# Optimization experiments

Hardware: AMD Instinct MI355X
Metric: run time of the kernel (lower is better)

## Reference

```python
import jax, jax.numpy as jnp
import numpy as np

B, N, M, D = 64, 16384, 64, 512
EPS = 1e-16


def setup_inputs() -> dict:
    key = jax.random.key(0)
    k1, k2, k3, k4 = jax.random.split(key, 4)
    controller_output = jax.random.normal(k1, (B, D), dtype=jnp.float32)
    w_prev = jax.random.uniform(k2, (B, N), dtype=jnp.float32)
    memory = jax.random.normal(k3, (B, N, M), dtype=jnp.float32)
    W = jax.random.normal(k4, (M + 6, D), dtype=jnp.float32) * (1.0 / np.sqrt(D))
    b = jnp.zeros((M + 6,), dtype=jnp.float32)
    return {"controller_output": controller_output, "w_prev": w_prev,
            "memory": memory, "W": W, "b": b}


def reference(controller_output, w_prev, memory, W, b):
    # fc_read projection -> [B, M+6], split into k, beta, g, s, gamma
    o = controller_output @ W.T + b
    k = o[:, :M]                      # [B, M] content key
    beta = jax.nn.softplus(o[:, M:M + 1])        # [B, 1] key strength
    g = jax.nn.sigmoid(o[:, M + 1:M + 2])        # [B, 1] interpolation gate
    s = jax.nn.softmax(o[:, M + 2:M + 5], axis=1)  # [B, 3] shift weights
    gamma = 1.0 + jax.nn.softplus(o[:, M + 5:M + 6])  # [B, 1] sharpening

    # content addressing: cosine similarity between k and each memory row
    num = jnp.einsum('bm,bnm->bn', k, memory)                      # [B, N]
    denom = (jnp.linalg.norm(k, axis=1, keepdims=True)
             * jnp.linalg.norm(memory, axis=2) + EPS)              # [B, N]
    w_c = jax.nn.softmax(beta * (num / denom), axis=1)             # [B, N]

    # interpolation with previous weighting
    w_g = g * w_c + (1.0 - g) * w_prev                              # [B, N]

    # circular convolution shift over {-1, 0, +1}
    w_t = (s[:, 0:1] * jnp.roll(w_g, 1, axis=1)
           + s[:, 1:2] * w_g
           + s[:, 2:3] * jnp.roll(w_g, -1, axis=1))                 # [B, N]

    # sharpening
    w_pow = w_t ** gamma
    w = w_pow / (jnp.sum(w_pow, axis=1, keepdims=True) + EPS)       # [B, N]

    # read: weighted sum of memory rows
    r = jnp.einsum('bn,bnm->bm', w, memory)                         # [B, M]
    return (r, w)
```

## Files before the change

### kernel.cpp

```cpp
#include <hip/hip_runtime.h>
#include <math.h>

#define B 64
#define N 16384
#define MDIM 64
#define DDIM 512
#define EPSF 1e-16f

#define K_OFF      0
#define SCAL_OFF   (B*64)
#define SCORE_OFF  (SCAL_OFF + B*8)
#define PART_OFF   (SCORE_OFF + B*N)

__device__ __forceinline__ float rowsum16(float x) {
    float t;
    t = __int_as_float(__builtin_amdgcn_update_dpp(0, __float_as_int(x), 0x128, 0xF, 0xF, true)); x += t;
    t = __int_as_float(__builtin_amdgcn_update_dpp(0, __float_as_int(x), 0x124, 0xF, 0xF, true)); x += t;
    t = __int_as_float(__builtin_amdgcn_update_dpp(0, __float_as_int(x), 0x122, 0xF, 0xF, true)); x += t;
    t = __int_as_float(__builtin_amdgcn_update_dpp(0, __float_as_int(x), 0x121, 0xF, 0xF, true)); x += t;
    return x;
}

__global__ __launch_bounds__(256) void k1(const float* __restrict__ c,
                                          const float* __restrict__ W,
                                          const float* __restrict__ bias,
                                          float* __restrict__ ws) {
    int b = blockIdx.x;
    __shared__ float cs[DDIM];
    __shared__ float osh[72];
    int tid = threadIdx.x;
    for (int i = tid; i < DDIM; i += 256) cs[i] = c[b * DDIM + i];
    __syncthreads();
    int wave = tid >> 6, lane = tid & 63;
    for (int j = wave; j < MDIM + 6; j += 4) {
        const float* wr = W + (size_t)j * DDIM;
        float sum = 0.f;
        for (int d = lane; d < DDIM; d += 64) sum += cs[d] * wr[d];
        for (int off = 32; off > 0; off >>= 1) sum += __shfl_xor(sum, off);
        if (lane == 0) osh[j] = sum + bias[j];
    }
    __syncthreads();
    if (tid < 64) ws[K_OFF + b * 64 + tid] = osh[tid];
    if (wave == 0) {
        float v = osh[lane];
        float sq = v * v;
        for (int off = 32; off > 0; off >>= 1) sq += __shfl_xor(sq, off);
        if (lane == 0) {
            float kn = sqrtf(sq);
            float ob = osh[64], og = osh[65], os0 = osh[66], os1 = osh[67],
                  os2 = osh[68], ogm = osh[69];
            float beta  = fmaxf(ob, 0.f) + log1pf(expf(-fabsf(ob)));
            float g     = 1.f / (1.f + expf(-og));
            float mx    = fmaxf(os0, fmaxf(os1, os2));
            float e0 = expf(os0 - mx), e1 = expf(os1 - mx), e2 = expf(os2 - mx);
            float es = e0 + e1 + e2;
            float gamma = 1.f + fmaxf(ogm, 0.f) + log1pf(expf(-fabsf(ogm)));
            float* sc = ws + SCAL_OFF + b * 8;
            sc[0] = kn; sc[1] = beta; sc[2] = g;
            sc[3] = e0 / es; sc[4] = e1 / es; sc[5] = e2 / es;
            sc[6] = gamma;
        }
    }
}

__global__ __launch_bounds__(256) void k2(const float* __restrict__ mem,
                                          float* __restrict__ ws) {
    int b = blockIdx.x >> 5, chunk = blockIdx.x & 31;
    __shared__ float ks[64];
    __shared__ float kb[2];
    int tid = threadIdx.x;
    if (tid < 64) ks[tid] = ws[K_OFF + b * 64 + tid];
    if (tid == 64) kb[0] = ws[SCAL_OFF + b * 8 + 0];
    if (tid == 65) kb[1] = ws[SCAL_OFF + b * 8 + 1];
    __syncthreads();
    float kn = kb[0], beta = kb[1];
    int grp = tid >> 4, ll = tid & 15;
    float k0 = ks[ll * 4], k1v = ks[ll * 4 + 1], k2v = ks[ll * 4 + 2], k3v = ks[ll * 4 + 3];
    int row0 = chunk * 512;
    #pragma unroll 4
    for (int it = 0; it < 32; ++it) {
        int row = row0 + it * 16 + grp;
        float4 v = *reinterpret_cast<const float4*>(
            mem + ((size_t)b * N + row) * MDIM + ll * 4);
        float dot = v.x * k0 + v.y * k1v + v.z * k2v + v.w * k3v;
        float sq  = v.x * v.x + v.y * v.y + v.z * v.z + v.w * v.w;
        dot = rowsum16(dot);
        sq  = rowsum16(sq);
        if (ll == 0) {
            float denom = kn * sqrtf(sq) + EPSF;
            ws[SCORE_OFF + (size_t)b * N + row] = beta * (dot / denom);
        }
    }
}

__global__ __launch_bounds__(1024) void kw(const float* __restrict__ w_prev,
                                           const float* __restrict__ ws,
                                           float* __restrict__ w_out) {
    int b = blockIdx.x;
    __shared__ float wg[N];
    __shared__ float red[16];
    int tid = threadIdx.x, wave = tid >> 6, lane = tid & 63;
    const float* sc = ws + SCORE_OFF + (size_t)b * N;
    const float* sl = ws + SCAL_OFF + b * 8;
    float g = sl[2], s0 = sl[3], s1 = sl[4], s2 = sl[5], gamma = sl[6];
    const float* wp = w_prev + (size_t)b * N;

    float scv[16];
    float mx = -INFINITY;
    #pragma unroll
    for (int j = 0; j < 16; ++j) {
        scv[j] = sc[tid + 1024 * j];
        mx = fmaxf(mx, scv[j]);
    }
    #pragma unroll
    for (int off = 32; off > 0; off >>= 1) mx = fmaxf(mx, __shfl_xor(mx, off));
    if (lane == 0) red[wave] = mx;
    __syncthreads();
    mx = red[0];
    #pragma unroll
    for (int w2 = 1; w2 < 16; ++w2) mx = fmaxf(mx, red[w2]);
    __syncthreads();

    float s = 0.f;
    #pragma unroll
    for (int j = 0; j < 16; ++j) {
        scv[j] = __expf(scv[j] - mx);
        s += scv[j];
    }
    #pragma unroll
    for (int off = 32; off > 0; off >>= 1) s += __shfl_xor(s, off);
    if (lane == 0) red[wave] = s;
    __syncthreads();
    s = red[0];
    #pragma unroll
    for (int w2 = 1; w2 < 16; ++w2) s += red[w2];
    float inv = 1.f / s;
    __syncthreads();

    #pragma unroll
    for (int j = 0; j < 16; ++j) {
        int i = tid + 1024 * j;
        wg[i] = g * (scv[j] * inv) + (1.f - g) * wp[i];
    }
    __syncthreads();

    float pv[16];
    float sp = 0.f;
    #pragma unroll
    for (int j = 0; j < 16; ++j) {
        int i = tid + 1024 * j;
        float wt = s0 * wg[(i - 1) & (N - 1)] + s1 * wg[i] + s2 * wg[(i + 1) & (N - 1)];
        float p = __expf(gamma * __logf(wt));
        pv[j] = p;
        sp += p;
    }
    #pragma unroll
    for (int off = 32; off > 0; off >>= 1) sp += __shfl_xor(sp, off);
    if (lane == 0) red[wave] = sp;
    __syncthreads();
    float spTot = red[0];
    #pragma unroll
    for (int w2 = 1; w2 < 16; ++w2) spTot += red[w2];
    float invp = 1.f / (spTot + EPSF);

    #pragma unroll
    for (int j = 0; j < 16; ++j) {
        int i = tid + 1024 * j;
        w_out[(size_t)b * N + i] = pv[j] * invp;
    }
}

__global__ __launch_bounds__(256) void kr(const float* __restrict__ mem,
                                          const float* __restrict__ w,
                                          float* __restrict__ part) {
    int b = blockIdx.x >> 5, chunk = blockIdx.x & 31;
    int tid = threadIdx.x, grp = tid >> 4, ll = tid & 15;
    float4 acc = make_float4(0.f, 0.f, 0.f, 0.f);
    int row0 = chunk * 512;
    #pragma unroll 4
    for (int it = 0; it < 32; ++it) {
        int row = row0 + it * 16 + grp;
        float wv = w[(size_t)b * N + row];
        float4 v = *reinterpret_cast<const float4*>(
            mem + ((size_t)b * N + row) * MDIM + ll * 4);
        acc.x += wv * v.x; acc.y += wv * v.y; acc.z += wv * v.z; acc.w += wv * v.w;
    }
    __shared__ float lds[16][64];
    lds[grp][ll * 4 + 0] = acc.x;
    lds[grp][ll * 4 + 1] = acc.y;
    lds[grp][ll * 4 + 2] = acc.z;
    lds[grp][ll * 4 + 3] = acc.w;
    __syncthreads();
    if (tid < 64) {
        float sacc = 0.f;
        #pragma unroll
        for (int gi = 0; gi < 16; ++gi) sacc += lds[gi][tid];
        part[(size_t)blockIdx.x * 64 + tid] = sacc;
    }
}

__global__ __launch_bounds__(64) void krr(const float* __restrict__ part,
                                          float* __restrict__ r) {
    int b = blockIdx.x, m = threadIdx.x;
    float s = 0.f;
    #pragma unroll
    for (int c = 0; c < 32; ++c) s += part[((size_t)b * 32 + c) * 64 + m];
    r[b * 64 + m] = s;
}

extern "C" void kernel_launch(void* const* d_in, const int* in_sizes, int n_in,
                              void* d_out, int out_size, void* d_ws, size_t ws_size,
                              hipStream_t stream) {
    const float* c      = (const float*)d_in[0];
    const float* w_prev = (const float*)d_in[1];
    const float* mem    = (const float*)d_in[2];
    const float* W      = (const float*)d_in[3];
    const float* bias   = (const float*)d_in[4];
    float* out = (float*)d_out;
    float* r_out = out;
    float* w_out = out + B * MDIM;
    float* ws = (float*)d_ws;

    k1<<<B, 256, 0, stream>>>(c, W, bias, ws);
    k2<<<B * 32, 256, 0, stream>>>(mem, ws);
    kw<<<B, 1024, 0, stream>>>(w_prev, ws, w_out);
    kr<<<B * 32, 256, 0, stream>>>(mem, w_out, ws + PART_OFF);
    krr<<<B, 64, 0, stream>>>(ws + PART_OFF, r_out);
}
```

Baseline: 113.7 us.

## Split per-batch softmax/sharpen kernel into chunked multi-block passes with tiny reduction kernels

Replaces the single 64-block kw kernel (one 1024-thread block per batch with 64KB LDS) with a chunked scheme. k2 now emits per-chunk max/sum-exp partials, and kc merges them with an online-softmax combine. kwb computes the interpolation, shift and power over 2048 blocks using a haloed LDS tile, kpp reduces the power sums, and kr folds the final normalization into the read pass and rescales w in place. This spreads the serial per-batch work across many CUs, at the cost of two extra launches and an extra read-modify-write of w. It also raises the k2 and kr unroll factor to 8.

```diff
diff --git a/kernel.cpp b/kernel.cpp
--- a/kernel.cpp
+++ b/kernel.cpp
@@ -10,7 +10,11 @@
 #define K_OFF      0
 #define SCAL_OFF   (B*64)
 #define SCORE_OFF  (SCAL_OFF + B*8)
-#define PART_OFF   (SCORE_OFF + B*N)
+#define MS_OFF     (SCORE_OFF + B*N)
+#define MXI_OFF    (MS_OFF + B*64)
+#define PSUM_OFF   (MXI_OFF + B*2)
+#define INVP_OFF   (PSUM_OFF + B*32)
+#define PART_OFF   (INVP_OFF + B)
 
 __device__ __forceinline__ float rowsum16(float x) {
     float t;
@@ -67,19 +71,21 @@
                                           float* __restrict__ ws) {
     int b = blockIdx.x >> 5, chunk = blockIdx.x & 31;
     __shared__ float ks[64];
-    __shared__ float kb[2];
+    __shared__ float kb2[2];
+    __shared__ float scbuf[512];
     int tid = threadIdx.x;
     if (tid < 64) ks[tid] = ws[K_OFF + b * 64 + tid];
-    if (tid == 64) kb[0] = ws[SCAL_OFF + b * 8 + 0];
-    if (tid == 65) kb[1] = ws[SCAL_OFF + b * 8 + 1];
-    __syncthreads();
-    float kn = kb[0], beta = kb[1];
+    if (tid == 64) kb2[0] = ws[SCAL_OFF + b * 8 + 0];
+    if (tid == 65) kb2[1] = ws[SCAL_OFF + b * 8 + 1];
+    __syncthreads();
+    float kn = kb2[0], beta = kb2[1];
     int grp = tid >> 4, ll = tid & 15;
     float k0 = ks[ll * 4], k1v = ks[ll * 4 + 1], k2v = ks[ll * 4 + 2], k3v = ks[ll * 4 + 3];
     int row0 = chunk * 512;
-    #pragma unroll 4
+    #pragma unroll 8
     for (int it = 0; it < 32; ++it) {
-        int row = row0 + it * 16 + grp;
+        int lrow = it * 16 + grp;
+        int row = row0 + lrow;
         float4 v = *reinterpret_cast<const float4*>(
             mem + ((size_t)b * N + row) * MDIM + ll * 4);
         float dot = v.x * k0 + v.y * k1v + v.z * k2v + v.w * k3v;
@@ -87,110 +93,140 @@
         dot = rowsum16(dot);
         sq  = rowsum16(sq);
         if (ll == 0) {
-            float denom = kn * sqrtf(sq) + EPSF;
-            ws[SCORE_OFF + (size_t)b * N + row] = beta * (dot / denom);
-        }
-    }
-}
-
-__global__ __launch_bounds__(1024) void kw(const float* __restrict__ w_prev,
-                                           const float* __restrict__ ws,
+            float score = beta * (dot / (kn * sqrtf(sq) + EPSF));
+            ws[SCORE_OFF + (size_t)b * N + row] = score;
+            scbuf[lrow] = score;
+        }
+    }
+    __syncthreads();
+    if (tid < 64) {
+        float vr[8];
+        float m = -1e30f;
+        #pragma unroll
+        for (int j = 0; j < 8; ++j) {
+            vr[j] = scbuf[tid + 64 * j];
+            m = fmaxf(m, vr[j]);
+        }
+        #pragma unroll
+        for (int off = 32; off > 0; off >>= 1) m = fmaxf(m, __shfl_xor(m, off));
+        float s = 0.f;
+        #pragma unroll
+        for (int j = 0; j < 8; ++j) s += __expf(vr[j] - m);
+        #pragma unroll
+        for (int off = 32; off > 0; off >>= 1) s += __shfl_xor(s, off);
+        if (tid == 0) {
+            ws[MS_OFF + ((size_t)b * 32 + chunk) * 2]     = m;
+            ws[MS_OFF + ((size_t)b * 32 + chunk) * 2 + 1] = s;
+        }
+    }
+}
+
+__global__ __launch_bounds__(64) void kc(float* __restrict__ ws) {
+    int b = blockIdx.x, lane = threadIdx.x;
+    float m = -1e30f, s = 0.f;
+    if (lane < 32) {
+        m = ws[MS_OFF + ((size_t)b * 32 + lane) * 2];
+        s = ws[MS_OFF + ((size_t)b * 32 + lane) * 2 + 1];
+    }
+    #pragma unroll
+    for (int off = 32; off > 0; off >>= 1) {
+        float m2 = __shfl_xor(m, off), s2 = __shfl_xor(s, off);
+        float M = fmaxf(m, m2);
+        s = s * __expf(m - M) + s2 * __expf(m2 - M);
+        m = M;
+    }
+    if (lane == 0) {
+        ws[MXI_OFF + b * 2]     = m;
+        ws[MXI_OFF + b * 2 + 1] = 1.f / s;
+    }
+}
+
+__global__ __launch_bounds__(256) void kwb(const float* __restrict__ w_prev,
+                                           float* __restrict__ ws,
                                            float* __restrict__ w_out) {
-    int b = blockIdx.x;
-    __shared__ float wg[N];
-    __shared__ float red[16];
+    int b = blockIdx.x >> 5, chunk = blockIdx.x & 31;
     int tid = threadIdx.x, wave = tid >> 6, lane = tid & 63;
-    const float* sc = ws + SCORE_OFF + (size_t)b * N;
+    __shared__ float wgL[514];
+    __shared__ float red[4];
     const float* sl = ws + SCAL_OFF + b * 8;
     float g = sl[2], s0 = sl[3], s1 = sl[4], s2 = sl[5], gamma = sl[6];
+    float mx  = ws[MXI_OFF + b * 2];
+    float inv = ws[MXI_OFF + b * 2 + 1];
+    const float* sc = ws + SCORE_OFF + (size_t)b * N;
     const float* wp = w_prev + (size_t)b * N;
-
-    float scv[16];
-    float mx = -INFINITY;
-    #pragma unroll
-    for (int j = 0; j < 16; ++j) {
-        scv[j] = sc[tid + 1024 * j];
-        mx = fmaxf(mx, scv[j]);
-    }
-    #pragma unroll
-    for (int off = 32; off > 0; off >>= 1) mx = fmaxf(mx, __shfl_xor(mx, off));
-    if (lane == 0) red[wave] = mx;
-    __syncthreads();
-    mx = red[0];
-    #pragma unroll
-    for (int w2 = 1; w2 < 16; ++w2) mx = fmaxf(mx, red[w2]);
-    __syncthreads();
-
-    float s = 0.f;
-    #pragma unroll
-    for (int j = 0; j < 16; ++j) {
-        scv[j] = __expf(scv[j] - mx);
-        s += scv[j];
-    }
-    #pragma unroll
-    for (int off = 32; off > 0; off >>= 1) s += __shfl_xor(s, off);
-    if (lane == 0) red[wave] = s;
-    __syncthreads();
-    s = red[0];
-    #pragma unroll
-    for (int w2 = 1; w2 < 16; ++w2) s += red[w2];
-    float inv = 1.f / s;
-    __syncthreads();
-
-    #pragma unroll
-    for (int j = 0; j < 16; ++j) {
-        int i = tid + 1024 * j;
-        wg[i] = g * (scv[j] * inv) + (1.f - g) * wp[i];
-    }
-    __syncthreads();
-
-    float pv[16];
-    float sp = 0.f;
-    #pragma unroll
-    for (int j = 0; j < 16; ++j) {
-        int i = tid + 1024 * j;
-        float wt = s0 * wg[(i - 1) & (N - 1)] + s1 * wg[i] + s2 * wg[(i + 1) & (N - 1)];
-        float p = __expf(gamma * __logf(wt));
-        pv[j] = p;
-        sp += p;
-    }
+    int row0 = chunk * 512;
+
+    {
+        int r0 = row0 + tid;
+        wgL[tid + 1]   = g * (__expf(sc[r0] - mx) * inv) + (1.f - g) * wp[r0];
+        int r1 = row0 + tid + 256;
+        wgL[tid + 257] = g * (__expf(sc[r1] - mx) * inv) + (1.f - g) * wp[r1];
+        if (tid == 0) {
+            int rl = (row0 - 1) & (N - 1);
+            wgL[0] = g * (__expf(sc[rl] - mx) * inv) + (1.f - g) * wp[rl];
+        }
+        if (tid == 255) {
+            int rr = (row0 + 512) & (N - 1);
+            wgL[513] = g * (__expf(sc[rr] - mx) * inv) + (1.f - g) * wp[rr];
+        }
+    }
+    __syncthreads();
+
+    float wt0 = s0 * wgL[tid]       + s1 * wgL[tid + 1]   + s2 * wgL[tid + 2];
+    float wt1 = s0 * wgL[tid + 256] + s1 * wgL[tid + 257] + s2 * wgL[tid + 258];
+    float p0 = __expf(gamma * __logf(wt0));
+    float p1 = __expf(gamma * __logf(wt1));
+    float* wo = w_out + (size_t)b * N + row0;
+    wo[tid]       = p0;
+    wo[tid + 256] = p1;
+
+    float sp = p0 + p1;
     #pragma unroll
     for (int off = 32; off > 0; off >>= 1) sp += __shfl_xor(sp, off);
     if (lane == 0) red[wave] = sp;
     __syncthreads();
-    float spTot = red[0];
-    #pragma unroll
-    for (int w2 = 1; w2 < 16; ++w2) spTot += red[w2];
-    float invp = 1.f / (spTot + EPSF);
-
-    #pragma unroll
-    for (int j = 0; j < 16; ++j) {
-        int i = tid + 1024 * j;
-        w_out[(size_t)b * N + i] = pv[j] * invp;
-    }
+    if (tid == 0)
+        ws[PSUM_OFF + b * 32 + chunk] = red[0] + red[1] + red[2] + red[3];
+}
+
+__global__ __launch_bounds__(64) void kpp(float* __restrict__ ws) {
+    int b = blockIdx.x, lane = threadIdx.x;
+    float s = (lane < 32) ? ws[PSUM_OFF + b * 32 + lane] : 0.f;
+    #pragma unroll
+    for (int off = 32; off > 0; off >>= 1) s += __shfl_xor(s, off);
+    if (lane == 0) ws[INVP_OFF + b] = 1.f / (s + EPSF);
 }
 
 __global__ __launch_bounds__(256) void kr(const float* __restrict__ mem,
-                                          const float* __restrict__ w,
+                                          float* __restrict__ w_out,
+                                          const float* __restrict__ ws,
                                           float* __restrict__ part) {
     int b = blockIdx.x >> 5, chunk = blockIdx.x & 31;
     int tid = threadIdx.x, grp = tid >> 4, ll = tid & 15;
+    float invp = ws[INVP_OFF + b];
+    float* wpow = w_out + (size_t)b * N;
     float4 acc = make_float4(0.f, 0.f, 0.f, 0.f);
     int row0 = chunk * 512;
-    #pragma unroll 4
+    #pragma unroll 8
     for (int it = 0; it < 32; ++it) {
         int row = row0 + it * 16 + grp;
-        float wv = w[(size_t)b * N + row];
+        float wv = wpow[row];
         float4 v = *reinterpret_cast<const float4*>(
             mem + ((size_t)b * N + row) * MDIM + ll * 4);
         acc.x += wv * v.x; acc.y += wv * v.y; acc.z += wv * v.z; acc.w += wv * v.w;
     }
     __shared__ float lds[16][64];
-    lds[grp][ll * 4 + 0] = acc.x;
-    lds[grp][ll * 4 + 1] = acc.y;
-    lds[grp][ll * 4 + 2] = acc.z;
-    lds[grp][ll * 4 + 3] = acc.w;
-    __syncthreads();
+    lds[grp][ll * 4 + 0] = acc.x * invp;
+    lds[grp][ll * 4 + 1] = acc.y * invp;
+    lds[grp][ll * 4 + 2] = acc.z * invp;
+    lds[grp][ll * 4 + 3] = acc.w * invp;
+    __syncthreads();
+    {
+        float a0 = wpow[row0 + tid] * invp;
+        float a1 = wpow[row0 + tid + 256] * invp;
+        wpow[row0 + tid]       = a0;
+        wpow[row0 + tid + 256] = a1;
+    }
     if (tid < 64) {
         float sacc = 0.f;
         #pragma unroll
@@ -221,9 +257,11 @@
     float* w_out = out + B * MDIM;
     float* ws = (float*)d_ws;
 
-    k1<<<B, 256, 0, stream>>>(c, W, bias, ws);
-    k2<<<B * 32, 256, 0, stream>>>(mem, ws);
-    kw<<<B, 1024, 0, stream>>>(w_prev, ws, w_out);
-    kr<<<B * 32, 256, 0, stream>>>(mem, w_out, ws + PART_OFF);
-    krr<<<B, 64, 0, stream>>>(ws + PART_OFF, r_out);
-}
+    k1 <<<B,      256, 0, stream>>>(c, W, bias, ws);
+    k2 <<<B * 32, 256, 0, stream>>>(mem, ws);
+    kc <<<B,       64, 0, stream>>>(ws);
+    kwb<<<B * 32, 256, 0, stream>>>(w_prev, ws, w_out);
+    kpp<<<B,       64, 0, stream>>>(ws);
+    kr <<<B * 32, 256, 0, stream>>>(mem, w_out, ws, ws + PART_OFF);
+    krr<<<B,       64, 0, stream>>>(ws + PART_OFF, r_out);
+}
```

New measurement: 116.6 us. +2.6%, slower.
